# Performance work log

Hardware: AMD Instinct MI355X
Metric: run time of the kernel (lower is better)

## Reference

```python
import jax, jax.numpy as jnp
import numpy as np

B, T, K = 512, 512, 64  # batch, seq_len, num_tags


def setup_inputs() -> dict:
    key = jax.random.key(0)
    k1, k2 = jax.random.split(key)
    inputs = jax.random.normal(k1, (B, T, K), dtype=jnp.float32)
    # learned CRF transition matrix (GlorotUniform-ish scale)
    transitions = jax.random.normal(k2, (K, K), dtype=jnp.float32) * 0.1
    return {"inputs": inputs, "transitions": transitions}


def _viterbi_decode(potentials, transitions, seq_lens):
    """Faithful jax version of tfa/tf crf_decode (max-plus Viterbi DP + backtrace).

    potentials: [B, T, K] unary scores
    transitions: [K, K] pairwise scores (from_tag, to_tag)
    seq_lens: [B] int valid lengths
    Returns (decode_tags [B, T] int32, best_score [B] float).
    """
    b, t, k = potentials.shape
    pots_t = jnp.transpose(potentials, (1, 0, 2))  # [T, B, K]
    # mask[t-1, b] = step t (1..T-1) is within sequence b
    mask = jnp.arange(1, t)[:, None] < seq_lens[None, :]  # [T-1, B]
    ident = jnp.arange(k, dtype=jnp.int32)

    def fwd_step(alpha, xs):
        pot_t, m = xs  # pot_t: [B, K], m: [B]
        scores = alpha[:, :, None] + transitions[None, :, :]  # [B, K_from, K_to]
        new_alpha = pot_t + jnp.max(scores, axis=1)           # [B, K]
        bp = jnp.argmax(scores, axis=1).astype(jnp.int32)     # [B, K]
        alpha = jnp.where(m[:, None], new_alpha, alpha)       # freeze past seq end
        bp = jnp.where(m[:, None], bp, ident[None, :])        # identity backptr
        return alpha, bp

    alpha0 = pots_t[0]
    alpha_final, bps = jax.lax.scan(fwd_step, alpha0, (pots_t[1:], mask))  # bps: [T-1, B, K]
    best_score = jnp.max(alpha_final, axis=1)                  # [B]
    last_tag = jnp.argmax(alpha_final, axis=1).astype(jnp.int32)  # [B]

    def back_step(tag, bp_t):
        prev = jnp.take_along_axis(bp_t, tag[:, None], axis=1)[:, 0]
        return prev, prev

    # reverse scan: ys[t] = best tag at time t, for t = 0..T-2
    _, prev_tags = jax.lax.scan(back_step, last_tag, bps, reverse=True)
    tags = jnp.concatenate([prev_tags, last_tag[None]], axis=0)  # [T, B]
    return jnp.transpose(tags), best_score


def reference(inputs, transitions):
    # sequence lengths derived exactly as in the original call()
    used = jnp.sign(jnp.abs(inputs))                       # [B, T, K]
    seq_lens = jnp.mean(jnp.sum(used, axis=1), axis=1)     # [B]
    seq_lens = seq_lens.astype(jnp.int32)
    decode_tags, _best_score = _viterbi_decode(inputs, transitions, seq_lens)
    return decode_tags
```

## Files before the change

### kernel.cpp

```cpp
#include <hip/hip_runtime.h>

#define BB 512
#define TT 512
#define KK 64

typedef float v2f __attribute__((ext_vector_type(2)));

__device__ __forceinline__ float frl(float v, int lane) {
    return __int_as_float(__builtin_amdgcn_readlane(__float_as_int(v), lane));
}
__device__ __forceinline__ v2f vmax2(v2f a, v2f b) {
    v2f r; r.x = fmaxf(a.x, b.x); r.y = fmaxf(a.y, b.y); return r;
}
__device__ __forceinline__ unsigned wave_umax63(unsigned x) {
    unsigned d;
    d = (unsigned)__builtin_amdgcn_update_dpp((int)x, (int)x, 0x111, 0xF, 0xF, false); x = x > d ? x : d;
    d = (unsigned)__builtin_amdgcn_update_dpp((int)x, (int)x, 0x112, 0xF, 0xF, false); x = x > d ? x : d;
    d = (unsigned)__builtin_amdgcn_update_dpp((int)x, (int)x, 0x114, 0xF, 0xF, false); x = x > d ? x : d;
    d = (unsigned)__builtin_amdgcn_update_dpp((int)x, (int)x, 0x118, 0xF, 0xF, false); x = x > d ? x : d;
    d = (unsigned)__builtin_amdgcn_update_dpp((int)x, (int)x, 0x142, 0xA, 0xF, false); x = x > d ? x : d;
    d = (unsigned)__builtin_amdgcn_update_dpp((int)x, (int)x, 0x143, 0xC, 0xF, false); x = x > d ? x : d;
    return x;
}

#define FSTEP(PT, TC) do {                                                      \
    la[lane] = alpha;                                                           \
    asm volatile("" ::: "memory");                                              \
    v2f acc0, acc1, acc2, acc3;                                                 \
    {                                                                           \
        float4 a4 = ((float4*)la)[0];                                           \
        v2f lo; lo.x = a4.x; lo.y = a4.y; acc0 = lo + tcl[0];                   \
        v2f hi; hi.x = a4.z; hi.y = a4.w; acc1 = hi + tch[0];                   \
        a4 = ((float4*)la)[1];                                                  \
        lo.x = a4.x; lo.y = a4.y; acc2 = lo + tcl[1];                           \
        hi.x = a4.z; hi.y = a4.w; acc3 = hi + tch[1];                           \
    }                                                                           \
    _Pragma("unroll")                                                           \
    for (int c = 2; c < 16; c += 2) {                                           \
        float4 a4 = ((float4*)la)[c];                                           \
        v2f lo; lo.x = a4.x; lo.y = a4.y; acc0 = vmax2(acc0, lo + tcl[c]);      \
        v2f hi; hi.x = a4.z; hi.y = a4.w; acc1 = vmax2(acc1, hi + tch[c]);      \
        a4 = ((float4*)la)[c + 1];                                              \
        lo.x = a4.x; lo.y = a4.y; acc2 = vmax2(acc2, lo + tcl[c + 1]);          \
        hi.x = a4.z; hi.y = a4.w; acc3 = vmax2(acc3, hi + tch[c + 1]);          \
    }                                                                           \
    v2f mm = vmax2(vmax2(acc0, acc1), vmax2(acc2, acc3));                       \
    float M = fmaxf(mm.x, mm.y);                                                \
    alpha = (TC) ? (PT + M) : alpha;                                            \
    *hp = alpha; hp += KK;                                                      \
} while (0)

__global__ __launch_bounds__(64, 1) void crf_fused(const float* __restrict__ pot,
                                                   const float* __restrict__ trans,
                                                   float* __restrict__ alphaH,
                                                   int* __restrict__ out) {
    __shared__ float tT[KK][KK + 1];
    __shared__ float la[KK];

    const int b = blockIdx.x;
    const int lane = threadIdx.x;
    const float* pb = pot + (size_t)b * TT * KK;
    float* hb = alphaH + (size_t)b * TT * KK;
    int* ob = out + b * TT;

    int cnt = 0;
    {
        const float4* p4 = (const float4*)pb;
        #pragma unroll 4
        for (int r = 0; r < 128; ++r) {
            float4 v = p4[lane + 64 * r];
            cnt += (v.x != 0.f) + (v.y != 0.f) + (v.z != 0.f) + (v.w != 0.f);
        }
        #pragma unroll
        for (int off = 32; off > 0; off >>= 1) cnt += __shfl_xor(cnt, off, 64);
    }
    const int seqlen = cnt >> 6;

    #pragma unroll 8
    for (int r = 0; r < KK; ++r) tT[lane][r] = trans[r * KK + lane];

    v2f tcl[16], tch[16];
    #pragma unroll
    for (int c = 0; c < 16; ++c) {
        v2f l2, h2;
        l2.x = trans[(4 * c + 0) * KK + lane]; l2.y = trans[(4 * c + 1) * KK + lane];
        h2.x = trans[(4 * c + 2) * KK + lane]; h2.y = trans[(4 * c + 3) * KK + lane];
        tcl[c] = l2; tch[c] = h2;
    }
    #pragma unroll
    for (int c = 0; c < 16; ++c) {
        asm volatile("" : "+v"(tcl[c]));
        asm volatile("" : "+v"(tch[c]));
    }

    float alpha = pb[lane];
    hb[lane] = alpha;
    float* hp = hb + KK + lane;

    float pf[4] = { pb[1 * KK + lane], pb[2 * KK + lane], pb[3 * KK + lane], pb[4 * KK + lane] };
    const float* lp = pb + 5 * KK + lane;

    int t = 1;
    #pragma unroll 1
    for (int c = 0; c < 126; ++c) {
        #pragma unroll
        for (int u = 0; u < 4; ++u) {
            FSTEP(pf[u], t < seqlen);
            pf[u] = *lp; lp += KK;
            ++t;
        }
    }
    float e0 = pb[509 * KK + lane], e1 = pb[510 * KK + lane], e2 = pb[511 * KK + lane];
    FSTEP(pf[0], 505 < seqlen);
    FSTEP(pf[1], 506 < seqlen);
    FSTEP(pf[2], 507 < seqlen);
    FSTEP(pf[3], 508 < seqlen);
    FSTEP(e0, 509 < seqlen);
    FSTEP(e1, 510 < seqlen);
    FSTEP(e2, 511 < seqlen);

    asm volatile("s_waitcnt vmcnt(0)" ::: "memory");

    float v = alpha; int idx = lane;
    #pragma unroll
    for (int off = 1; off < 64; off <<= 1) {
        float vo = __shfl_xor(v, off, 64);
        int io = __shfl_xor(idx, off, 64);
        bool take = (vo > v) || (vo == v && io < idx);
        v = take ? vo : v;
        idx = take ? io : idx;
    }
    int cur = idx;
    int slot = cur;

    float r0 = hb[510 * KK + lane], r1 = hb[509 * KK + lane], r2 = hb[508 * KK + lane],
          r3 = hb[507 * KK + lane], r4 = hb[506 * KK + lane], r5 = hb[505 * KK + lane],
          r6 = hb[504 * KK + lane], r7 = hb[503 * KK + lane];

    auto bt_step = [&](int tt, float arow) {
        if (tt < seqlen) {
            float cand = arow + tT[cur][lane];
            unsigned u = __float_as_uint(cand);
            u = u ^ ((unsigned)(((int)u) >> 31) | 0x80000000u);
            unsigned run = wave_umax63(u);
            unsigned Umax = (unsigned)__builtin_amdgcn_readlane((int)run, 63);
            unsigned long long mk = __ballot(u == Umax);
            cur = (int)__builtin_ctzll(mk);
        }
        const int tm = tt - 1;
        slot = ((tm & 63) == lane) ? cur : slot;
        if ((tm & 63) == 0) ob[tm + lane] = slot;
    };

    int T0 = 511;
    for (int c = 0; c < 63; ++c) {
        bt_step(T0 - 0, r0); { int pi = T0 - 9;  pi = pi < 0 ? 0 : pi; r0 = hb[pi * KK + lane]; }
        bt_step(T0 - 1, r1); { int pi = T0 - 10; pi = pi < 0 ? 0 : pi; r1 = hb[pi * KK + lane]; }
        bt_step(T0 - 2, r2); { int pi = T0 - 11; pi = pi < 0 ? 0 : pi; r2 = hb[pi * KK + lane]; }
        bt_step(T0 - 3, r3); { int pi = T0 - 12; pi = pi < 0 ? 0 : pi; r3 = hb[pi * KK + lane]; }
        bt_step(T0 - 4, r4); { int pi = T0 - 13; pi = pi < 0 ? 0 : pi; r4 = hb[pi * KK + lane]; }
        bt_step(T0 - 5, r5); { int pi = T0 - 14; pi = pi < 0 ? 0 : pi; r5 = hb[pi * KK + lane]; }
        bt_step(T0 - 6, r6); { int pi = T0 - 15; pi = pi < 0 ? 0 : pi; r6 = hb[pi * KK + lane]; }
        bt_step(T0 - 7, r7); { int pi = T0 - 16; pi = pi < 0 ? 0 : pi; r7 = hb[pi * KK + lane]; }
        T0 -= 8;
    }
    bt_step(7, r0); bt_step(6, r1); bt_step(5, r2); bt_step(4, r3);
    bt_step(3, r4); bt_step(2, r5); bt_step(1, r6);
}

__global__ __launch_bounds__(256) void seqlen_kernel(const float* __restrict__ inp,
                                                     int* __restrict__ seq_lens) {
    int b = blockIdx.x;
    int tid = threadIdx.x;
    const float4* p4 = (const float4*)(inp + (size_t)b * TT * KK);
    const int n4 = TT * KK / 4;
    int cnt = 0;
    for (int idx = tid; idx < n4; idx += 256) {
        float4 v = p4[idx];
        cnt += (v.x != 0.0f) + (v.y != 0.0f) + (v.z != 0.0f) + (v.w != 0.0f);
    }
    #pragma unroll
    for (int off = 32; off > 0; off >>= 1) cnt += __shfl_down(cnt, off, 64);
    __shared__ int wsum[4];
    if ((tid & 63) == 0) wsum[tid >> 6] = cnt;
    __syncthreads();
    if (tid == 0) seq_lens[b] = (wsum[0] + wsum[1] + wsum[2] + wsum[3]) >> 6;
}

__global__ __launch_bounds__(64) void viterbi_fallback(const float* __restrict__ pot,
                                                       const float* __restrict__ trans,
                                                       const int* __restrict__ seq_lens,
                                                       int* __restrict__ out) {
    __shared__ unsigned char bp[TT][KK];
    const int b = blockIdx.x;
    const int j = threadIdx.x;

    float tc[KK];
    #pragma unroll
    for (int i = 0; i < KK; ++i) tc[i] = trans[i * KK + j];

    const float* pb = pot + (size_t)b * TT * KK;
    float alpha = pb[j];
    const int seqlen = seq_lens[b];

    for (int t = 1; t < TT; ++t) {
        float ptj = pb[t * KK + j];
        float m[4]; int am[4];
        #pragma unroll
        for (int c = 0; c < 4; ++c) {
            const int i = c * 16;
            float ai = frl(alpha, i);
            m[c] = ai + tc[i];
            am[c] = i;
        }
        #pragma unroll
        for (int q = 1; q < 16; ++q) {
            #pragma unroll
            for (int c = 0; c < 4; ++c) {
                const int i = c * 16 + q;
                float ai = frl(alpha, i);
                float s = ai + tc[i];
                bool g = s > m[c];
                m[c] = g ? s : m[c];
                am[c] = g ? i : am[c];
            }
        }
        float M = m[0]; int BI = am[0];
        #pragma unroll
        for (int c = 1; c < 4; ++c) {
            bool g = m[c] > M;
            M = g ? m[c] : M;
            BI = g ? am[c] : BI;
        }
        const bool valid = (t < seqlen);
        alpha = valid ? (ptj + M) : alpha;
        bp[t][j] = (unsigned char)(valid ? BI : j);
    }

    float v = alpha; int idx = j;
    #pragma unroll
    for (int off = 1; off < 64; off <<= 1) {
        float vo = __shfl_xor(v, off, 64);
        int io = __shfl_xor(idx, off, 64);
        bool take = (vo > v) || (vo == v && io < idx);
        v = take ? vo : v;
        idx = take ? io : idx;
    }
    __syncthreads();
    if (j == 0) {
        int* ob = out + b * TT;
        int cur = idx;
        ob[TT - 1] = cur;
        for (int p = TT - 2; p >= 0; --p) {
            cur = bp[p + 1][cur];
            ob[p] = cur;
        }
    }
}

extern "C" void kernel_launch(void* const* d_in, const int* in_sizes, int n_in,
                              void* d_out, int out_size, void* d_ws, size_t ws_size,
                              hipStream_t stream) {
    const float* inp = (const float*)d_in[0];
    const float* trans = (const float*)d_in[1];
    int* out = (int*)d_out;

    const size_t histBytes = (size_t)BB * TT * KK * sizeof(float);
    if (ws_size >= histBytes) {
        float* alphaH = (float*)d_ws;
        crf_fused<<<BB, 64, 0, stream>>>(inp, trans, alphaH, out);
    } else {
        int* seq = (int*)d_ws;
        seqlen_kernel<<<BB, 256, 0, stream>>>(inp, seq);
        viterbi_fallback<<<BB, KK, 0, stream>>>(inp, trans, seq, out);
    }
}
```

Before: 282.4 us.

## Process two batch sequences per wavefront to interleave independent Viterbi chains

Each single-wave block now handles two batch rows at once, interleaving both forward max-plus recurrences and both backtraces so the two independent dependency chains can hide each other's LDS and reduction latency. The grid is halved to 256 blocks. On a part with more CUs than blocks, this cuts parallelism across CUs and roughly doubles per-wave register and instruction work, so the instruction-level overlap has to outweigh the lost parallelism.

```diff
diff --git a/kernel.cpp b/kernel.cpp
--- a/kernel.cpp
+++ b/kernel.cpp
@@ -23,58 +23,77 @@
     return x;
 }
 
-#define FSTEP(PT, TC) do {                                                      \
-    la[lane] = alpha;                                                           \
+#define NEG_INF (-3.402823466e+38f)
+
+#define FSTEP2(PT0, PT1, TC0, TC1) do {                                         \
+    la0[lane] = alpha0;                                                         \
+    la1[lane] = alpha1;                                                         \
     asm volatile("" ::: "memory");                                              \
-    v2f acc0, acc1, acc2, acc3;                                                 \
-    {                                                                           \
-        float4 a4 = ((float4*)la)[0];                                           \
-        v2f lo; lo.x = a4.x; lo.y = a4.y; acc0 = lo + tcl[0];                   \
-        v2f hi; hi.x = a4.z; hi.y = a4.w; acc1 = hi + tch[0];                   \
-        a4 = ((float4*)la)[1];                                                  \
-        lo.x = a4.x; lo.y = a4.y; acc2 = lo + tcl[1];                           \
-        hi.x = a4.z; hi.y = a4.w; acc3 = hi + tch[1];                           \
+    v2f A0, A1, A2, A3, B0, B1, B2, B3;                                         \
+    A0 = A1 = A2 = A3 = (v2f){NEG_INF, NEG_INF};                                \
+    B0 = B1 = B2 = B3 = (v2f){NEG_INF, NEG_INF};                                \
+    _Pragma("unroll")                                                           \
+    for (int c = 0; c < 16; c += 2) {                                           \
+        float4 xa = ((float4*)la0)[c];                                          \
+        float4 xb = ((float4*)la1)[c];                                          \
+        float4 ya = ((float4*)la0)[c + 1];                                      \
+        float4 yb = ((float4*)la1)[c + 1];                                      \
+        v2f lo, hi;                                                             \
+        lo.x = xa.x; lo.y = xa.y; A0 = vmax2(A0, lo + tcl[c]);                  \
+        hi.x = xa.z; hi.y = xa.w; A1 = vmax2(A1, hi + tch[c]);                  \
+        lo.x = xb.x; lo.y = xb.y; B0 = vmax2(B0, lo + tcl[c]);                  \
+        hi.x = xb.z; hi.y = xb.w; B1 = vmax2(B1, hi + tch[c]);                  \
+        lo.x = ya.x; lo.y = ya.y; A2 = vmax2(A2, lo + tcl[c + 1]);              \
+        hi.x = ya.z; hi.y = ya.w; A3 = vmax2(A3, hi + tch[c + 1]);              \
+        lo.x = yb.x; lo.y = yb.y; B2 = vmax2(B2, lo + tcl[c + 1]);              \
+        hi.x = yb.z; hi.y = yb.w; B3 = vmax2(B3, hi + tch[c + 1]);              \
     }                                                                           \
-    _Pragma("unroll")                                                           \
-    for (int c = 2; c < 16; c += 2) {                                           \
-        float4 a4 = ((float4*)la)[c];                                           \
-        v2f lo; lo.x = a4.x; lo.y = a4.y; acc0 = vmax2(acc0, lo + tcl[c]);      \
-        v2f hi; hi.x = a4.z; hi.y = a4.w; acc1 = vmax2(acc1, hi + tch[c]);      \
-        a4 = ((float4*)la)[c + 1];                                              \
-        lo.x = a4.x; lo.y = a4.y; acc2 = vmax2(acc2, lo + tcl[c + 1]);          \
-        hi.x = a4.z; hi.y = a4.w; acc3 = vmax2(acc3, hi + tch[c + 1]);          \
-    }                                                                           \
-    v2f mm = vmax2(vmax2(acc0, acc1), vmax2(acc2, acc3));                       \
-    float M = fmaxf(mm.x, mm.y);                                                \
-    alpha = (TC) ? (PT + M) : alpha;                                            \
-    *hp = alpha; hp += KK;                                                      \
+    v2f ma = vmax2(vmax2(A0, A1), vmax2(A2, A3));                               \
+    v2f mb = vmax2(vmax2(B0, B1), vmax2(B2, B3));                               \
+    float M0 = fmaxf(ma.x, ma.y);                                               \
+    float M1 = fmaxf(mb.x, mb.y);                                               \
+    alpha0 = (TC0) ? (PT0 + M0) : alpha0;                                       \
+    alpha1 = (TC1) ? (PT1 + M1) : alpha1;                                       \
+    *hp0 = alpha0; hp0 += KK;                                                   \
+    *hp1 = alpha1; hp1 += KK;                                                   \
 } while (0)
 
-__global__ __launch_bounds__(64, 1) void crf_fused(const float* __restrict__ pot,
-                                                   const float* __restrict__ trans,
-                                                   float* __restrict__ alphaH,
-                                                   int* __restrict__ out) {
+__global__ __launch_bounds__(64, 1) void crf_fused2(const float* __restrict__ pot,
+                                                    const float* __restrict__ trans,
+                                                    float* __restrict__ alphaH,
+                                                    int* __restrict__ out) {
     __shared__ float tT[KK][KK + 1];
-    __shared__ float la[KK];
-
-    const int b = blockIdx.x;
+    __shared__ float la0[KK], la1[KK];
+
+    const int b0 = blockIdx.x * 2;
+    const int b1 = b0 + 1;
     const int lane = threadIdx.x;
-    const float* pb = pot + (size_t)b * TT * KK;
-    float* hb = alphaH + (size_t)b * TT * KK;
-    int* ob = out + b * TT;
-
-    int cnt = 0;
+    const float* pb0 = pot + (size_t)b0 * TT * KK;
+    const float* pb1 = pot + (size_t)b1 * TT * KK;
+    float* hb0 = alphaH + (size_t)b0 * TT * KK;
+    float* hb1 = alphaH + (size_t)b1 * TT * KK;
+    int* ob0 = out + b0 * TT;
+    int* ob1 = out + b1 * TT;
+
+    int cnt0 = 0, cnt1 = 0;
     {
-        const float4* p4 = (const float4*)pb;
+        const float4* p40 = (const float4*)pb0;
+        const float4* p41 = (const float4*)pb1;
         #pragma unroll 4
         for (int r = 0; r < 128; ++r) {
-            float4 v = p4[lane + 64 * r];
-            cnt += (v.x != 0.f) + (v.y != 0.f) + (v.z != 0.f) + (v.w != 0.f);
-        }
-        #pragma unroll
-        for (int off = 32; off > 0; off >>= 1) cnt += __shfl_xor(cnt, off, 64);
-    }
-    const int seqlen = cnt >> 6;
+            float4 v = p40[lane + 64 * r];
+            float4 u = p41[lane + 64 * r];
+            cnt0 += (v.x != 0.f) + (v.y != 0.f) + (v.z != 0.f) + (v.w != 0.f);
+            cnt1 += (u.x != 0.f) + (u.y != 0.f) + (u.z != 0.f) + (u.w != 0.f);
+        }
+        #pragma unroll
+        for (int off = 32; off > 0; off >>= 1) {
+            cnt0 += __shfl_xor(cnt0, off, 64);
+            cnt1 += __shfl_xor(cnt1, off, 64);
+        }
+    }
+    const int seqlen0 = cnt0 >> 6;
+    const int seqlen1 = cnt1 >> 6;
 
     #pragma unroll 8
     for (int r = 0; r < KK; ++r) tT[lane][r] = trans[r * KK + lane];
@@ -93,79 +112,117 @@
         asm volatile("" : "+v"(tch[c]));
     }
 
-    float alpha = pb[lane];
-    hb[lane] = alpha;
-    float* hp = hb + KK + lane;
-
-    float pf[4] = { pb[1 * KK + lane], pb[2 * KK + lane], pb[3 * KK + lane], pb[4 * KK + lane] };
-    const float* lp = pb + 5 * KK + lane;
+    float alpha0 = pb0[lane], alpha1 = pb1[lane];
+    hb0[lane] = alpha0; hb1[lane] = alpha1;
+    float* hp0 = hb0 + KK + lane;
+    float* hp1 = hb1 + KK + lane;
+
+    float pa[4] = { pb0[1*KK+lane], pb0[2*KK+lane], pb0[3*KK+lane], pb0[4*KK+lane] };
+    float qa[4] = { pb1[1*KK+lane], pb1[2*KK+lane], pb1[3*KK+lane], pb1[4*KK+lane] };
+    const float* lp0 = pb0 + 5 * KK + lane;
+    const float* lp1 = pb1 + 5 * KK + lane;
 
     int t = 1;
     #pragma unroll 1
     for (int c = 0; c < 126; ++c) {
         #pragma unroll
         for (int u = 0; u < 4; ++u) {
-            FSTEP(pf[u], t < seqlen);
-            pf[u] = *lp; lp += KK;
+            FSTEP2(pa[u], qa[u], t < seqlen0, t < seqlen1);
+            pa[u] = *lp0; lp0 += KK;
+            qa[u] = *lp1; lp1 += KK;
             ++t;
         }
     }
-    float e0 = pb[509 * KK + lane], e1 = pb[510 * KK + lane], e2 = pb[511 * KK + lane];
-    FSTEP(pf[0], 505 < seqlen);
-    FSTEP(pf[1], 506 < seqlen);
-    FSTEP(pf[2], 507 < seqlen);
-    FSTEP(pf[3], 508 < seqlen);
-    FSTEP(e0, 509 < seqlen);
-    FSTEP(e1, 510 < seqlen);
-    FSTEP(e2, 511 < seqlen);
+    {
+        float e0 = pb0[509*KK+lane], e1 = pb0[510*KK+lane], e2 = pb0[511*KK+lane];
+        float f0 = pb1[509*KK+lane], f1 = pb1[510*KK+lane], f2 = pb1[511*KK+lane];
+        FSTEP2(pa[0], qa[0], 505 < seqlen0, 505 < seqlen1);
+        FSTEP2(pa[1], qa[1], 506 < seqlen0, 506 < seqlen1);
+        FSTEP2(pa[2], qa[2], 507 < seqlen0, 507 < seqlen1);
+        FSTEP2(pa[3], qa[3], 508 < seqlen0, 508 < seqlen1);
+        FSTEP2(e0, f0, 509 < seqlen0, 509 < seqlen1);
+        FSTEP2(e1, f1, 510 < seqlen0, 510 < seqlen1);
+        FSTEP2(e2, f2, 511 < seqlen0, 511 < seqlen1);
+    }
 
     asm volatile("s_waitcnt vmcnt(0)" ::: "memory");
 
-    float v = alpha; int idx = lane;
-    #pragma unroll
-    for (int off = 1; off < 64; off <<= 1) {
-        float vo = __shfl_xor(v, off, 64);
-        int io = __shfl_xor(idx, off, 64);
-        bool take = (vo > v) || (vo == v && io < idx);
-        v = take ? vo : v;
-        idx = take ? io : idx;
-    }
-    int cur = idx;
-    int slot = cur;
-
-    float r0 = hb[510 * KK + lane], r1 = hb[509 * KK + lane], r2 = hb[508 * KK + lane],
-          r3 = hb[507 * KK + lane], r4 = hb[506 * KK + lane], r5 = hb[505 * KK + lane],
-          r6 = hb[504 * KK + lane], r7 = hb[503 * KK + lane];
-
-    auto bt_step = [&](int tt, float arow) {
-        if (tt < seqlen) {
-            float cand = arow + tT[cur][lane];
+    int cur0, cur1;
+    {
+        float v = alpha0; int idx = lane;
+        #pragma unroll
+        for (int off = 1; off < 64; off <<= 1) {
+            float vo = __shfl_xor(v, off, 64);
+            int io = __shfl_xor(idx, off, 64);
+            bool take = (vo > v) || (vo == v && io < idx);
+            v = take ? vo : v; idx = take ? io : idx;
+        }
+        cur0 = idx;
+    }
+    {
+        float v = alpha1; int idx = lane;
+        #pragma unroll
+        for (int off = 1; off < 64; off <<= 1) {
+            float vo = __shfl_xor(v, off, 64);
+            int io = __shfl_xor(idx, off, 64);
+            bool take = (vo > v) || (vo == v && io < idx);
+            v = take ? vo : v; idx = take ? io : idx;
+        }
+        cur1 = idx;
+    }
+    int slot0 = cur0, slot1 = cur1;
+
+    float ra[8], rb[8];
+    #pragma unroll
+    for (int k = 0; k < 8; ++k) {
+        ra[k] = hb0[(510 - k) * KK + lane];
+        rb[k] = hb1[(510 - k) * KK + lane];
+    }
+
+    auto bt2 = [&](int tt, float arow, float brow) {
+        unsigned u0 = 0, u1 = 0;
+        bool d0 = (tt < seqlen0), d1 = (tt < seqlen1);
+        if (d0) {
+            float cand = arow + tT[cur0][lane];
             unsigned u = __float_as_uint(cand);
-            u = u ^ ((unsigned)(((int)u) >> 31) | 0x80000000u);
-            unsigned run = wave_umax63(u);
+            u0 = u ^ ((unsigned)(((int)u) >> 31) | 0x80000000u);
+        }
+        if (d1) {
+            float cand = brow + tT[cur1][lane];
+            unsigned u = __float_as_uint(cand);
+            u1 = u ^ ((unsigned)(((int)u) >> 31) | 0x80000000u);
+        }
+        if (d0) {
+            unsigned run = wave_umax63(u0);
             unsigned Umax = (unsigned)__builtin_amdgcn_readlane((int)run, 63);
-            unsigned long long mk = __ballot(u == Umax);
-            cur = (int)__builtin_ctzll(mk);
+            unsigned long long mk = __ballot(u0 == Umax);
+            cur0 = (int)__builtin_ctzll(mk);
+        }
+        if (d1) {
+            unsigned run = wave_umax63(u1);
+            unsigned Umax = (unsigned)__builtin_amdgcn_readlane((int)run, 63);
+            unsigned long long mk = __ballot(u1 == Umax);
+            cur1 = (int)__builtin_ctzll(mk);
         }
         const int tm = tt - 1;
-        slot = ((tm & 63) == lane) ? cur : slot;
-        if ((tm & 63) == 0) ob[tm + lane] = slot;
+        slot0 = ((tm & 63) == lane) ? cur0 : slot0;
+        slot1 = ((tm & 63) == lane) ? cur1 : slot1;
+        if ((tm & 63) == 0) { ob0[tm + lane] = slot0; ob1[tm + lane] = slot1; }
     };
 
     int T0 = 511;
     for (int c = 0; c < 63; ++c) {
-        bt_step(T0 - 0, r0); { int pi = T0 - 9;  pi = pi < 0 ? 0 : pi; r0 = hb[pi * KK + lane]; }
-        bt_step(T0 - 1, r1); { int pi = T0 - 10; pi = pi < 0 ? 0 : pi; r1 = hb[pi * KK + lane]; }
-        bt_step(T0 - 2, r2); { int pi = T0 - 11; pi = pi < 0 ? 0 : pi; r2 = hb[pi * KK + lane]; }
-        bt_step(T0 - 3, r3); { int pi = T0 - 12; pi = pi < 0 ? 0 : pi; r3 = hb[pi * KK + lane]; }
-        bt_step(T0 - 4, r4); { int pi = T0 - 13; pi = pi < 0 ? 0 : pi; r4 = hb[pi * KK + lane]; }
-        bt_step(T0 - 5, r5); { int pi = T0 - 14; pi = pi < 0 ? 0 : pi; r5 = hb[pi * KK + lane]; }
-        bt_step(T0 - 6, r6); { int pi = T0 - 15; pi = pi < 0 ? 0 : pi; r6 = hb[pi * KK + lane]; }
-        bt_step(T0 - 7, r7); { int pi = T0 - 16; pi = pi < 0 ? 0 : pi; r7 = hb[pi * KK + lane]; }
+        #pragma unroll
+        for (int k = 0; k < 8; ++k) {
+            bt2(T0 - k, ra[k], rb[k]);
+            int pi = T0 - 9 - k; pi = pi < 0 ? 0 : pi;
+            ra[k] = hb0[pi * KK + lane];
+            rb[k] = hb1[pi * KK + lane];
+        }
         T0 -= 8;
     }
-    bt_step(7, r0); bt_step(6, r1); bt_step(5, r2); bt_step(4, r3);
-    bt_step(3, r4); bt_step(2, r5); bt_step(1, r6);
+    #pragma unroll
+    for (int k = 0; k < 7; ++k) bt2(7 - k, ra[k], rb[k]);
 }
 
 __global__ __launch_bounds__(256) void seqlen_kernel(const float* __restrict__ inp,
@@ -268,7 +325,7 @@
     const size_t histBytes = (size_t)BB * TT * KK * sizeof(float);
     if (ws_size >= histBytes) {
         float* alphaH = (float*)d_ws;
-        crf_fused<<<BB, 64, 0, stream>>>(inp, trans, alphaH, out);
+        crf_fused2<<<BB / 2, 64, 0, stream>>>(inp, trans, alphaH, out);
     } else {
         int* seq = (int*)d_ws;
         seqlen_kernel<<<BB, 256, 0, stream>>>(inp, seq);
```

Result: slower. 526.1 us (+86.3%).

## Stage potentials into LDS via async global_load_lds double buffering

Applied to the files above, without the earlier changes.

Replaces per-step global loads of the potential rows in the serial forward Viterbi loop with a double-buffered LDS staging scheme. Rows arrive in 32-row chunks through global_load_lds, and the next chunk is issued every 32 timesteps. The aim is to take global-memory latency off the sequential dependency chain. The cost is extra LDS and full vmcnt waits, which also drain the outstanding history stores. Those waits could stall the loop, and the chunk-index arithmetic has to line up exactly with the step count.

```diff
diff --git a/kernel.cpp b/kernel.cpp
--- a/kernel.cpp
+++ b/kernel.cpp
@@ -21,6 +21,11 @@
     d = (unsigned)__builtin_amdgcn_update_dpp((int)x, (int)x, 0x142, 0xA, 0xF, false); x = x > d ? x : d;
     d = (unsigned)__builtin_amdgcn_update_dpp((int)x, (int)x, 0x143, 0xC, 0xF, false); x = x > d ? x : d;
     return x;
+}
+
+__device__ __forceinline__ void gl_lds16(const float* g, float* l) {
+    __builtin_amdgcn_global_load_lds((const __attribute__((address_space(1))) void*)g,
+                                     (__attribute__((address_space(3))) void*)l, 16, 0, 0);
 }
 
 #define FSTEP(PT, TC) do {                                                      \
@@ -56,12 +61,18 @@
                                                    int* __restrict__ out) {
     __shared__ float tT[KK][KK + 1];
     __shared__ float la[KK];
+    __shared__ float stage[2][32 * KK];
 
     const int b = blockIdx.x;
     const int lane = threadIdx.x;
     const float* pb = pot + (size_t)b * TT * KK;
     float* hb = alphaH + (size_t)b * TT * KK;
     int* ob = out + b * TT;
+
+    #pragma unroll
+    for (int k = 0; k < 8; ++k) gl_lds16(pb + k * 256 + lane * 4, &stage[0][k * 256]);
+    #pragma unroll
+    for (int k = 0; k < 8; ++k) gl_lds16(pb + 2048 + k * 256 + lane * 4, &stage[1][k * 256]);
 
     int cnt = 0;
     {
@@ -93,31 +104,49 @@
         asm volatile("" : "+v"(tch[c]));
     }
 
-    float alpha = pb[lane];
+    asm volatile("s_waitcnt vmcnt(0)" ::: "memory");
+
+    float alpha = stage[0][lane];
     hb[lane] = alpha;
     float* hp = hb + KK + lane;
 
-    float pf[4] = { pb[1 * KK + lane], pb[2 * KK + lane], pb[3 * KK + lane], pb[4 * KK + lane] };
-    const float* lp = pb + 5 * KK + lane;
+    float pf[4] = { stage[0][1 * KK + lane], stage[0][2 * KK + lane],
+                    stage[0][3 * KK + lane], stage[0][4 * KK + lane] };
 
     int t = 1;
     #pragma unroll 1
     for (int c = 0; c < 126; ++c) {
+        if ((c & 7) == 6) {
+            asm volatile("s_waitcnt vmcnt(0)" ::: "memory");
+        } else if ((c & 7) == 7) {
+            const int cn = ((1 + 4 * c) >> 5) + 2;
+            if (cn < 16) {
+                const float* g0 = pb + cn * 32 * KK;
+                float* l0 = &stage[cn & 1][0];
+                #pragma unroll
+                for (int k = 0; k < 8; ++k) gl_lds16(g0 + k * 256 + lane * 4, l0 + k * 256);
+            }
+        }
         #pragma unroll
         for (int u = 0; u < 4; ++u) {
             FSTEP(pf[u], t < seqlen);
-            pf[u] = *lp; lp += KK;
+            int rn = t + 4; rn = rn > 511 ? 511 : rn;
+            pf[u] = stage[(rn >> 5) & 1][(rn & 31) * KK + lane];
             ++t;
         }
     }
-    float e0 = pb[509 * KK + lane], e1 = pb[510 * KK + lane], e2 = pb[511 * KK + lane];
     FSTEP(pf[0], 505 < seqlen);
     FSTEP(pf[1], 506 < seqlen);
     FSTEP(pf[2], 507 < seqlen);
     FSTEP(pf[3], 508 < seqlen);
-    FSTEP(e0, 509 < seqlen);
-    FSTEP(e1, 510 < seqlen);
-    FSTEP(e2, 511 < seqlen);
+    {
+        float e0 = stage[1][(509 & 31) * KK + lane];
+        float e1 = stage[1][(510 & 31) * KK + lane];
+        float e2 = stage[1][(511 & 31) * KK + lane];
+        FSTEP(e0, 509 < seqlen);
+        FSTEP(e1, 510 < seqlen);
+        FSTEP(e2, 511 < seqlen);
+    }
 
     asm volatile("s_waitcnt vmcnt(0)" ::: "memory");
 
```

Result: slower. 370.6 us (+31.2%).
